# Optimization experiments

Measured on AMD Instinct MI355X. Metric: run time of the kernel, lower is better.

Reference implementation:

```python
import jax, jax.numpy as jnp
import numpy as np

B, S, HID = 2, 2048, 1024
NH, HD = 16, 64  # num heads, head dim
NEG = 1e10

def setup_inputs() -> dict:
    key = jax.random.key(0)
    ks = jax.random.split(key, 4)
    scale = 1.0 / np.sqrt(HID)
    return {
        "hidden_states": jax.random.normal(ks[0], (B, S, HID), jnp.float32),
        "attention_mask": jnp.zeros((B, 1, 1, S), jnp.float32),
        "Wq": jax.random.normal(ks[1], (HID, HID), jnp.float32) * scale,
        "bq": jnp.zeros((HID,), jnp.float32),
        "Wk": jax.random.normal(ks[2], (HID, HID), jnp.float32) * scale,
        "bk": jnp.zeros((HID,), jnp.float32),
        "Wv": jax.random.normal(ks[3], (HID, HID), jnp.float32) * scale,
        "bv": jnp.zeros((HID,), jnp.float32),
    }

def _split_heads(x):
    # [B,S,HID] -> [B,NH,S,HD]
    return x.reshape(B, S, NH, HD).transpose(0, 2, 1, 3)

def reference(hidden_states, attention_mask, Wq, bq, Wk, bk, Wv, bv):
    q = _split_heads(hidden_states @ Wq.T + bq)
    k = _split_heads(hidden_states @ Wk.T + bk)
    v = _split_heads(hidden_states @ Wv.T + bv)
    scores = jnp.einsum("bhqd,bhkd->bhqk", q, k) / np.sqrt(HD)
    causal = jnp.tril(jnp.ones((S, S), jnp.float32))  # [S,S]
    scores = scores * causal - NEG * (1.0 - causal)
    scores = scores + attention_mask
    probs = jax.nn.softmax(scores, axis=-1)  # [B,NH,S,S]
    ctx = jnp.einsum("bhqk,bhkd->bhqd", probs, v)
    ctx = ctx.transpose(0, 2, 1, 3).reshape(B, S, HID)
    return (ctx, probs)
```

## Files before the change

kernel.cpp:

```cpp
#include <hip/hip_runtime.h>

#define S_LEN 2048
#define HIDN  1024
#define NHEAD 16
#define HDIM  64
#define NBATCH 2

typedef __bf16 bf16x8 __attribute__((ext_vector_type(8)));
typedef float  f32x4  __attribute__((ext_vector_type(4)));
typedef unsigned int  u32x4 __attribute__((ext_vector_type(4)));
typedef unsigned short u16;
typedef unsigned short u16x4 __attribute__((ext_vector_type(4)));

#define LOG2E      1.4426950408889634f
#define QS_L2E     0.18033688011112042f
#define NEG8_L2E  -11.541560327111707f

#define PSTR 68

__device__ __forceinline__ u16 f2bf(float f) {
    union { float f; unsigned int u; } v; v.f = f;
    unsigned int u = v.u;
    unsigned int r = ((u >> 16) & 1u) + 0x7FFFu;
    return (u16)((u + r) >> 16);
}

__device__ __forceinline__ f32x4 mfma16(bf16x8 a, bf16x8 b, f32x4 c) {
    return __builtin_amdgcn_mfma_f32_16x16x32_bf16(a, b, c, 0, 0, 0);
}

__device__ __forceinline__ f32x4 zf4() { f32x4 z = {0.f, 0.f, 0.f, 0.f}; return z; }

__device__ __forceinline__ bf16x8 pack8_trunc(f32x4 a, f32x4 b) {
    union { f32x4 f; u32x4 u; } ua, ub;
    ua.f = a; ub.f = b;
    union { unsigned int d[4]; bf16x8 v; } r;
    r.d[0] = __builtin_amdgcn_perm(ua.u.y, ua.u.x, 0x07060302u);
    r.d[1] = __builtin_amdgcn_perm(ua.u.w, ua.u.z, 0x07060302u);
    r.d[2] = __builtin_amdgcn_perm(ub.u.y, ub.u.x, 0x07060302u);
    r.d[3] = __builtin_amdgcn_perm(ub.u.w, ub.u.z, 0x07060302u);
    return r.v;
}

__device__ __forceinline__ void gld16(void* lds, const void* g) {
    __builtin_amdgcn_global_load_lds(
        (const __attribute__((address_space(1))) void*)g,
        (__attribute__((address_space(3))) void*)lds, 16, 0, 0);
}

__global__ __launch_bounds__(256) void cvt_all(
    const float* __restrict__ hs, const float* __restrict__ Wq,
    const float* __restrict__ Wk, const float* __restrict__ Wv,
    u16* __restrict__ hsb, u16* __restrict__ Wqb,
    u16* __restrict__ Wkb, u16* __restrict__ Wvb)
{
    const int NBH = (NBATCH * S_LEN * HIDN) / 1024;
    const int NBW = (HIDN * HIDN) / 1024;
    int bid = blockIdx.x;
    const float* __restrict__ s; u16* __restrict__ d;
    if (bid < NBH)                { s = hs; d = hsb; }
    else if (bid < NBH + NBW)     { s = Wq; d = Wqb; bid -= NBH; }
    else if (bid < NBH + 2 * NBW) { s = Wk; d = Wkb; bid -= NBH + NBW; }
    else                          { s = Wv; d = Wvb; bid -= NBH + 2 * NBW; }
    const int i = (bid * 256 + (int)threadIdx.x) * 4;
    float4 v = *(const float4*)&s[i];
    u16x4 o = { f2bf(v.x), f2bf(v.y), f2bf(v.z), f2bf(v.w) };
    *(u16x4*)&d[i] = o;
}

__global__ __launch_bounds__(256) void qkv_fused(
    const u16* __restrict__ hsb,
    const u16* __restrict__ Wqb, const u16* __restrict__ Wkb, const u16* __restrict__ Wvb,
    const float* __restrict__ bq, const float* __restrict__ bk, const float* __restrict__ bv,
    u16* __restrict__ Qf, u16* __restrict__ Kf, u16* __restrict__ Vt)
{
    __shared__ u16 As[128 * 64];
    __shared__ u16 Bs[3][64 * 64];

    const int mbase = blockIdx.x * 128;
    const int nbase = blockIdx.y * 64;
    const int tid  = threadIdx.x;
    const int lane = tid & 63;
    const int wv   = tid >> 6;
    const int wm   = wv >> 1, wn = wv & 1;
    const int lrow = lane & 15, quad = lane >> 4;
    const int l7   = lrow & 7;

    const u16* __restrict__ Wm[3] = { Wqb, Wkb, Wvb };

    const u16* ap[4];
#pragma unroll
    for (int t = 0; t < 4; ++t) {
        const int c = tid + t * 256;
        const int r = c >> 3;
        const int o = ((c & 7) ^ (r & 7)) * 8;
        ap[t] = &hsb[(size_t)(mbase + r) * HIDN + o];
    }
    const u16* bp[3][2];
#pragma unroll
    for (int z = 0; z < 3; ++z)
#pragma unroll
        for (int t = 0; t < 2; ++t) {
            const int c = tid + t * 256;
            const int r = c >> 3;
            const int o = ((c & 7) ^ (r & 7)) * 8;
            bp[z][t] = &Wm[z][(size_t)(nbase + r) * HIDN + o];
        }

    f32x4 accqk[2][2][4];
    f32x4 accv[4][2];
#pragma unroll
    for (int z = 0; z < 2; ++z)
#pragma unroll
        for (int j = 0; j < 2; ++j)
#pragma unroll
            for (int i = 0; i < 4; ++i) accqk[z][j][i] = zf4();
#pragma unroll
    for (int i = 0; i < 4; ++i)
#pragma unroll
        for (int j = 0; j < 2; ++j) accv[i][j] = zf4();

    for (int k0 = 0; k0 < HIDN; k0 += 64) {
#pragma unroll
        for (int t = 0; t < 4; ++t)
            gld16(&As[(tid + t * 256) * 8], ap[t] + k0);
#pragma unroll
        for (int z = 0; z < 3; ++z)
#pragma unroll
            for (int t = 0; t < 2; ++t)
                gld16(&Bs[z][(tid + t * 256) * 8], bp[z][t] + k0);
        __syncthreads();

#pragma unroll
        for (int kk = 0; kk < 2; ++kk) {
            const int sc = ((kk * 4 + quad) ^ l7) * 8;
            bf16x8 hf[4], wf[3][2];
#pragma unroll
            for (int i = 0; i < 4; ++i)
                hf[i] = *(const bf16x8*)&As[(wm * 64 + i * 16 + lrow) * 64 + sc];
#pragma unroll
            for (int z = 0; z < 3; ++z)
#pragma unroll
                for (int j = 0; j < 2; ++j)
                    wf[z][j] = *(const bf16x8*)&Bs[z][(wn * 32 + j * 16 + lrow) * 64 + sc];
#pragma unroll
            for (int z = 0; z < 2; ++z)
#pragma unroll
                for (int j = 0; j < 2; ++j)
#pragma unroll
                    for (int i = 0; i < 4; ++i)
                        accqk[z][j][i] = mfma16(wf[z][j], hf[i], accqk[z][j][i]);
#pragma unroll
            for (int i = 0; i < 4; ++i)
#pragma unroll
                for (int j = 0; j < 2; ++j)
                    accv[i][j] = mfma16(hf[i], wf[2][j], accv[i][j]);
        }
        __syncthreads();
    }

#pragma unroll
    for (int z = 0; z < 2; ++z) {
        u16* __restrict__ O = (z == 0) ? Qf : Kf;
        const float* __restrict__ bias = (z == 0) ? bq : bk;
#pragma unroll
        for (int j = 0; j < 2; ++j) {
#pragma unroll
            for (int i = 0; i < 4; ++i) {
                const int n0 = nbase + wn * 32 + j * 16 + quad * 4;
                const int m  = mbase + wm * 64 + i * 16 + lrow;
                const float4 b4 = *(const float4*)&bias[n0];
                u16x4 pk = { f2bf(accqk[z][j][i][0] + b4.x), f2bf(accqk[z][j][i][1] + b4.y),
                             f2bf(accqk[z][j][i][2] + b4.z), f2bf(accqk[z][j][i][3] + b4.w) };
                *(u16x4*)&O[(size_t)m * HIDN + n0] = pk;
            }
        }
    }
    {
        const int bb = mbase >> 11;
        const int sb = mbase & 2047;
#pragma unroll
        for (int i = 0; i < 4; ++i) {
#pragma unroll
            for (int j = 0; j < 2; ++j) {
                const int n = nbase + wn * 32 + j * 16 + lrow;
                const int hh = n >> 6, d = n & 63;
                const float bs = bv[n];
                const int s0 = sb + wm * 64 + i * 16 + quad * 4;
                u16x4 pk = { f2bf(accv[i][j][0] + bs), f2bf(accv[i][j][1] + bs),
                             f2bf(accv[i][j][2] + bs), f2bf(accv[i][j][3] + bs) };
                *(u16x4*)&Vt[(((size_t)(bb * NHEAD + hh)) * HDIM + d) * S_LEN + s0] = pk;
            }
        }
    }
}

__global__ __launch_bounds__(256) void attn_kernel(
    const u16* __restrict__ Qf,
    const u16* __restrict__ Kf,
    const u16* __restrict__ Vt,
    const float* __restrict__ amask,
    float* __restrict__ ctx,
    float* __restrict__ probs)
{
    const int qt = 127 - blockIdx.x;
    const int h  = blockIdx.y;
    const int b  = blockIdx.z;
    const int bh = b * NHEAD + h;
    const int tid  = threadIdx.x;
    const int lane = tid & 63;
    const int wv   = tid >> 6;
    const int lrow = lane & 15, quad = lane >> 4;
    const int row0 = qt * 16;
    const int dti  = qt >> 2;
    const int nkt  = dti + 1;

    __shared__ float pfl[4][16 * PSTR];
    __shared__ float l_sh[4][16];

    {
        const int tail  = nkt * 64;
        const int nt4   = (S_LEN - tail) >> 2;
        const int r  = tid >> 4;
        const int c0 = tid & 15;
        const f32x4 zf = {0.f, 0.f, 0.f, 0.f};
        float* pr = &probs[((size_t)bh * S_LEN + row0 + r) * S_LEN + tail];
        for (int c4 = c0; c4 < nt4; c4 += 16)
            __builtin_nontemporal_store(zf, (f32x4*)&pr[c4 * 4]);
    }

    const u16* qp = &Qf[((size_t)b * S_LEN + row0 + lrow) * HIDN + h * HDIM + quad * 8];
    const bf16x8 qa0 = *(const bf16x8*)qp;
    const bf16x8 qa1 = *(const bf16x8*)(qp + 32);

    const float* __restrict__ am = &amask[(size_t)b * S_LEN];
    const u16* __restrict__ kbase = &Kf[(size_t)b * S_LEN * HIDN + h * HDIM + quad * 8];

    float l_lane[4] = {0.f, 0.f, 0.f, 0.f};
    for (int kt = wv; kt < nkt; kt += 4) {
        f32x4 c[4];
#pragma unroll
        for (int cb = 0; cb < 4; ++cb) {
            const int col = kt * 64 + cb * 16 + lrow;
            const u16* kp = kbase + (size_t)col * HIDN;
            bf16x8 kb0 = *(const bf16x8*)kp;
            bf16x8 kb1 = *(const bf16x8*)(kp + 32);
            c[cb] = mfma16(qa0, kb0, zf4());
            c[cb] = mfma16(qa1, kb1, c[cb]);
        }
        if (kt == dti) {
#pragma unroll
            for (int cb = 0; cb < 4; ++cb) {
                const int col = kt * 64 + cb * 16 + lrow;
                const float m8 = fmaf(am[col], LOG2E, NEG8_L2E);
#pragma unroll
                for (int reg = 0; reg < 4; ++reg) {
                    const int row = row0 + quad * 4 + reg;
                    const float e = exp2f(fmaf(c[cb][reg], QS_L2E, m8));
                    l_lane[reg] += (col <= row) ? e : 0.f;
                }
            }
        } else {
#pragma unroll
            for (int cb = 0; cb < 4; ++cb) {
                const int col = kt * 64 + cb * 16 + lrow;
                const float m8 = fmaf(am[col], LOG2E, NEG8_L2E);
#pragma unroll
                for (int reg = 0; reg < 4; ++reg)
                    l_lane[reg] += exp2f(fmaf(c[cb][reg], QS_L2E, m8));
            }
        }
    }
#pragma unroll
    for (int reg = 0; reg < 4; ++reg) {
#pragma unroll
        for (int off = 1; off < 16; off <<= 1)
            l_lane[reg] += __shfl_xor(l_lane[reg], off, 16);
    }
    if (lrow == 0) {
#pragma unroll
        for (int reg = 0; reg < 4; ++reg)
            l_sh[wv][quad * 4 + reg] = l_lane[reg];
    }
    __syncthreads();
    float inv_l[4];
#pragma unroll
    for (int reg = 0; reg < 4; ++reg) {
        const int rr = quad * 4 + reg;
        inv_l[reg] = 1.f / (l_sh[0][rr] + l_sh[1][rr] + l_sh[2][rr] + l_sh[3][rr]);
    }

    f32x4 av[4];
#pragma unroll
    for (int db = 0; db < 4; ++db) av[db] = zf4();

    float* __restrict__ pw = pfl[wv];
    const u16* __restrict__ vbase = &Vt[(size_t)bh * HDIM * S_LEN + quad * 8];

    for (int kt = wv; kt < nkt; kt += 4) {
        f32x4 c[4];
#pragma unroll
        for (int cb = 0; cb < 4; ++cb) {
            const int col = kt * 64 + cb * 16 + lrow;
            const u16* kp = kbase + (size_t)col * HIDN;
            bf16x8 kb0 = *(const bf16x8*)kp;
            bf16x8 kb1 = *(const bf16x8*)(kp + 32);
            c[cb] = mfma16(qa0, kb0, zf4());
            c[cb] = mfma16(qa1, kb1, c[cb]);
        }
        if (kt == dti) {
#pragma unroll
            for (int cb = 0; cb < 4; ++cb) {
                const int col = kt * 64 + cb * 16 + lrow;
                const float m8 = fmaf(am[col], LOG2E, NEG8_L2E);
#pragma unroll
                for (int reg = 0; reg < 4; ++reg) {
                    const int row = row0 + quad * 4 + reg;
                    const float p = (col <= row)
                        ? exp2f(fmaf(c[cb][reg], QS_L2E, m8)) * inv_l[reg] : 0.f;
                    pw[(quad * 4 + reg) * PSTR + cb * 16 + lrow] = p;
                }
            }
        } else {
#pragma unroll
            for (int cb = 0; cb < 4; ++cb) {
                const int col = kt * 64 + cb * 16 + lrow;
                const float m8 = fmaf(am[col], LOG2E, NEG8_L2E);
#pragma unroll
                for (int reg = 0; reg < 4; ++reg) {
                    const float p = exp2f(fmaf(c[cb][reg], QS_L2E, m8)) * inv_l[reg];
                    pw[(quad * 4 + reg) * PSTR + cb * 16 + lrow] = p;
                }
            }
        }

#pragma unroll
        for (int it = 0; it < 4; ++it) {
            const int r = it * 4 + quad;
            f32x4 v = *(const f32x4*)&pw[r * PSTR + lrow * 4];
            __builtin_nontemporal_store(
                v, (f32x4*)&probs[((size_t)bh * S_LEN + row0 + r) * S_LEN + kt * 64 + lrow * 4]);
        }

        f32x4 p0 = *(const f32x4*)&pw[lrow * PSTR + quad * 8];
        f32x4 p1 = *(const f32x4*)&pw[lrow * PSTR + quad * 8 + 4];
        f32x4 p2 = *(const f32x4*)&pw[lrow * PSTR + 32 + quad * 8];
        f32x4 p3 = *(const f32x4*)&pw[lrow * PSTR + 32 + quad * 8 + 4];
        bf16x8 pa0 = pack8_trunc(p0, p1);
        bf16x8 pa1 = pack8_trunc(p2, p3);
#pragma unroll
        for (int db = 0; db < 4; ++db) {
            const u16* vp = vbase + (size_t)(db * 16 + lrow) * S_LEN + kt * 64;
            bf16x8 vb0 = *(const bf16x8*)vp;
            bf16x8 vb1 = *(const bf16x8*)(vp + 32);
            av[db] = mfma16(pa0, vb0, av[db]);
            av[db] = mfma16(pa1, vb1, av[db]);
        }
    }

#pragma unroll
    for (int db = 0; db < 4; ++db)
#pragma unroll
        for (int reg = 0; reg < 4; ++reg)
            pw[lane * 16 + ((db * 4 + reg + (lane >> 1)) & 15)] = av[db][reg];
    __syncthreads();
#pragma unroll
    for (int reg = 0; reg < 4; ++reg) {
        const int sl = lane * 16 + ((wv * 4 + reg + (lane >> 1)) & 15);
        const float s = pfl[0][sl] + pfl[1][sl] + pfl[2][sl] + pfl[3][sl];
        __builtin_nontemporal_store(
            s, &ctx[((size_t)b * S_LEN + row0 + quad * 4 + reg) * HIDN + h * HDIM + wv * 16 + lrow]);
    }
}

extern "C" void kernel_launch(void* const* d_in, const int* in_sizes, int n_in,
                              void* d_out, int out_size, void* d_ws, size_t ws_size,
                              hipStream_t stream)
{
    const float* hs    = (const float*)d_in[0];
    const float* amask = (const float*)d_in[1];
    const float* Wq    = (const float*)d_in[2];
    const float* bq    = (const float*)d_in[3];
    const float* Wk    = (const float*)d_in[4];
    const float* bk    = (const float*)d_in[5];
    const float* Wv    = (const float*)d_in[6];
    const float* bv    = (const float*)d_in[7];

    float* out   = (float*)d_out;
    float* ctx   = out;
    float* probs = out + (size_t)NBATCH * S_LEN * HIDN;

    const size_t NTOK = (size_t)NBATCH * S_LEN;
    u16* hsb = (u16*)d_ws;
    u16* Wqb = hsb + NTOK * HIDN;
    u16* Wkb = Wqb + (size_t)HIDN * HIDN;
    u16* Wvb = Wkb + (size_t)HIDN * HIDN;
    u16* Qf  = Wvb + (size_t)HIDN * HIDN;
    u16* Kf  = Qf + NTOK * HIDN;
    u16* Vt  = Kf + NTOK * HIDN;

    const int nblk_cvt = (int)(NTOK * HIDN / 1024) + 3 * (HIDN * HIDN / 1024);
    cvt_all<<<nblk_cvt, 256, 0, stream>>>(hs, Wq, Wk, Wv, hsb, Wqb, Wkb, Wvb);

    qkv_fused<<<dim3(32, 16), 256, 0, stream>>>(hsb, Wqb, Wkb, Wvb, bq, bk, bv, Qf, Kf, Vt);
    attn_kernel<<<dim3(128, 16, 2), 256, 0, stream>>>(Qf, Kf, Vt, amask, ctx, probs);
}
```

Before: 762.1 us.

## Cache bf16 exp scores in LDS to avoid recomputing QK^T in second pass

The first pass now stores unnormalized exponentials as bf16 in shared memory. The second pass reuses them to write normalized probabilities and feed the PV MFMA, instead of recomputing QK^T and exp. Normalization of the context is applied after accumulation. The launch is split into two kernels with different LDS footprints depending on how many key tiles each query tile needs. This trades large LDS use (lower occupancy) and bf16 rounding of stored probabilities for less compute and K-loading.

```diff
diff --git a/kernel.cpp b/kernel.cpp
--- a/kernel.cpp
+++ b/kernel.cpp
@@ -16,8 +16,6 @@
 #define QS_L2E     0.18033688011112042f
 #define NEG8_L2E  -11.541560327111707f
 
-#define PSTR 68
-
 __device__ __forceinline__ u16 f2bf(float f) {
     union { float f; unsigned int u; } v; v.f = f;
     unsigned int u = v.u;
@@ -25,22 +23,16 @@
     return (u16)((u + r) >> 16);
 }
 
+__device__ __forceinline__ float bf2f(u16 h) {
+    union { unsigned int u; float f; } v; v.u = ((unsigned int)h) << 16;
+    return v.f;
+}
+
 __device__ __forceinline__ f32x4 mfma16(bf16x8 a, bf16x8 b, f32x4 c) {
     return __builtin_amdgcn_mfma_f32_16x16x32_bf16(a, b, c, 0, 0, 0);
 }
 
 __device__ __forceinline__ f32x4 zf4() { f32x4 z = {0.f, 0.f, 0.f, 0.f}; return z; }
-
-__device__ __forceinline__ bf16x8 pack8_trunc(f32x4 a, f32x4 b) {
-    union { f32x4 f; u32x4 u; } ua, ub;
-    ua.f = a; ub.f = b;
-    union { unsigned int d[4]; bf16x8 v; } r;
-    r.d[0] = __builtin_amdgcn_perm(ua.u.y, ua.u.x, 0x07060302u);
-    r.d[1] = __builtin_amdgcn_perm(ua.u.w, ua.u.z, 0x07060302u);
-    r.d[2] = __builtin_amdgcn_perm(ub.u.y, ub.u.x, 0x07060302u);
-    r.d[3] = __builtin_amdgcn_perm(ub.u.w, ub.u.z, 0x07060302u);
-    return r.v;
-}
 
 __device__ __forceinline__ void gld16(void* lds, const void* g) {
     __builtin_amdgcn_global_load_lds(
@@ -195,15 +187,18 @@
     }
 }
 
-__global__ __launch_bounds__(256) void attn_kernel(
+template<int NC>
+__global__ __launch_bounds__(256) void attn_1p(
     const u16* __restrict__ Qf,
     const u16* __restrict__ Kf,
     const u16* __restrict__ Vt,
     const float* __restrict__ amask,
     float* __restrict__ ctx,
-    float* __restrict__ probs)
+    float* __restrict__ probs,
+    int qt_base)
 {
-    const int qt = 127 - blockIdx.x;
+    constexpr int STR = NC + 8;
+    const int qt = qt_base - (int)blockIdx.x;
     const int h  = blockIdx.y;
     const int b  = blockIdx.z;
     const int bh = b * NHEAD + h;
@@ -215,7 +210,7 @@
     const int dti  = qt >> 2;
     const int nkt  = dti + 1;
 
-    __shared__ float pfl[4][16 * PSTR];
+    __shared__ __align__(16) u16 expb[16 * STR];
     __shared__ float l_sh[4][16];
 
     {
@@ -256,8 +251,10 @@
 #pragma unroll
                 for (int reg = 0; reg < 4; ++reg) {
                     const int row = row0 + quad * 4 + reg;
-                    const float e = exp2f(fmaf(c[cb][reg], QS_L2E, m8));
-                    l_lane[reg] += (col <= row) ? e : 0.f;
+                    const float e = (col <= row)
+                        ? exp2f(fmaf(c[cb][reg], QS_L2E, m8)) : 0.f;
+                    l_lane[reg] += e;
+                    expb[(quad * 4 + reg) * STR + kt * 64 + cb * 16 + lrow] = f2bf(e);
                 }
             }
         } else {
@@ -266,8 +263,11 @@
                 const int col = kt * 64 + cb * 16 + lrow;
                 const float m8 = fmaf(am[col], LOG2E, NEG8_L2E);
 #pragma unroll
-                for (int reg = 0; reg < 4; ++reg)
-                    l_lane[reg] += exp2f(fmaf(c[cb][reg], QS_L2E, m8));
+                for (int reg = 0; reg < 4; ++reg) {
+                    const float e = exp2f(fmaf(c[cb][reg], QS_L2E, m8));
+                    l_lane[reg] += e;
+                    expb[(quad * 4 + reg) * STR + kt * 64 + cb * 16 + lrow] = f2bf(e);
+                }
             }
         }
     }
@@ -294,60 +294,22 @@
 #pragma unroll
     for (int db = 0; db < 4; ++db) av[db] = zf4();
 
-    float* __restrict__ pw = pfl[wv];
     const u16* __restrict__ vbase = &Vt[(size_t)bh * HDIM * S_LEN + quad * 8];
 
     for (int kt = wv; kt < nkt; kt += 4) {
-        f32x4 c[4];
-#pragma unroll
-        for (int cb = 0; cb < 4; ++cb) {
-            const int col = kt * 64 + cb * 16 + lrow;
-            const u16* kp = kbase + (size_t)col * HIDN;
-            bf16x8 kb0 = *(const bf16x8*)kp;
-            bf16x8 kb1 = *(const bf16x8*)(kp + 32);
-            c[cb] = mfma16(qa0, kb0, zf4());
-            c[cb] = mfma16(qa1, kb1, c[cb]);
-        }
-        if (kt == dti) {
-#pragma unroll
-            for (int cb = 0; cb < 4; ++cb) {
-                const int col = kt * 64 + cb * 16 + lrow;
-                const float m8 = fmaf(am[col], LOG2E, NEG8_L2E);
-#pragma unroll
-                for (int reg = 0; reg < 4; ++reg) {
-                    const int row = row0 + quad * 4 + reg;
-                    const float p = (col <= row)
-                        ? exp2f(fmaf(c[cb][reg], QS_L2E, m8)) * inv_l[reg] : 0.f;
-                    pw[(quad * 4 + reg) * PSTR + cb * 16 + lrow] = p;
-                }
-            }
-        } else {
-#pragma unroll
-            for (int cb = 0; cb < 4; ++cb) {
-                const int col = kt * 64 + cb * 16 + lrow;
-                const float m8 = fmaf(am[col], LOG2E, NEG8_L2E);
-#pragma unroll
-                for (int reg = 0; reg < 4; ++reg) {
-                    const float p = exp2f(fmaf(c[cb][reg], QS_L2E, m8)) * inv_l[reg];
-                    pw[(quad * 4 + reg) * PSTR + cb * 16 + lrow] = p;
-                }
-            }
-        }
-
 #pragma unroll
         for (int it = 0; it < 4; ++it) {
-            const int r = it * 4 + quad;
-            f32x4 v = *(const f32x4*)&pw[r * PSTR + lrow * 4];
+            const int r = quad * 4 + it;
+            const float inv = inv_l[it];
+            u16x4 p4 = *(const u16x4*)&expb[r * STR + kt * 64 + lrow * 4];
+            f32x4 o;
+#pragma unroll
+            for (int j = 0; j < 4; ++j) o[j] = bf2f(p4[j]) * inv;
             __builtin_nontemporal_store(
-                v, (f32x4*)&probs[((size_t)bh * S_LEN + row0 + r) * S_LEN + kt * 64 + lrow * 4]);
-        }
-
-        f32x4 p0 = *(const f32x4*)&pw[lrow * PSTR + quad * 8];
-        f32x4 p1 = *(const f32x4*)&pw[lrow * PSTR + quad * 8 + 4];
-        f32x4 p2 = *(const f32x4*)&pw[lrow * PSTR + 32 + quad * 8];
-        f32x4 p3 = *(const f32x4*)&pw[lrow * PSTR + 32 + quad * 8 + 4];
-        bf16x8 pa0 = pack8_trunc(p0, p1);
-        bf16x8 pa1 = pack8_trunc(p2, p3);
+                o, (f32x4*)&probs[((size_t)bh * S_LEN + row0 + r) * S_LEN + kt * 64 + lrow * 4]);
+        }
+        const bf16x8 pa0 = *(const bf16x8*)&expb[lrow * STR + kt * 64 + quad * 8];
+        const bf16x8 pa1 = *(const bf16x8*)&expb[lrow * STR + kt * 64 + 32 + quad * 8];
 #pragma unroll
         for (int db = 0; db < 4; ++db) {
             const u16* vp = vbase + (size_t)(db * 16 + lrow) * S_LEN + kt * 64;
@@ -357,17 +319,25 @@
             av[db] = mfma16(pa1, vb1, av[db]);
         }
     }
-
 #pragma unroll
     for (int db = 0; db < 4; ++db)
 #pragma unroll
         for (int reg = 0; reg < 4; ++reg)
-            pw[lane * 16 + ((db * 4 + reg + (lane >> 1)) & 15)] = av[db][reg];
+            av[db][reg] *= inv_l[reg];
+
     __syncthreads();
+    float* cmb = (float*)expb;
+#pragma unroll
+    for (int db = 0; db < 4; ++db)
+#pragma unroll
+        for (int reg = 0; reg < 4; ++reg)
+            cmb[wv * (64 * 17) + lane * 17 + db * 4 + reg] = av[db][reg];
+    __syncthreads();
 #pragma unroll
     for (int reg = 0; reg < 4; ++reg) {
-        const int sl = lane * 16 + ((wv * 4 + reg + (lane >> 1)) & 15);
-        const float s = pfl[0][sl] + pfl[1][sl] + pfl[2][sl] + pfl[3][sl];
+        const int sl = lane * 17 + wv * 4 + reg;
+        const float s = cmb[0 * (64 * 17) + sl] + cmb[1 * (64 * 17) + sl]
+                      + cmb[2 * (64 * 17) + sl] + cmb[3 * (64 * 17) + sl];
         __builtin_nontemporal_store(
             s, &ctx[((size_t)b * S_LEN + row0 + quad * 4 + reg) * HIDN + h * HDIM + wv * 16 + lrow]);
     }
@@ -403,5 +373,7 @@
     cvt_all<<<nblk_cvt, 256, 0, stream>>>(hs, Wq, Wk, Wv, hsb, Wqb, Wkb, Wvb);
 
     qkv_fused<<<dim3(32, 16), 256, 0, stream>>>(hsb, Wqb, Wkb, Wvb, bq, bk, bv, Qf, Kf, Vt);
-    attn_kernel<<<dim3(128, 16, 2), 256, 0, stream>>>(Qf, Kf, Vt, amask, ctx, probs);
-}
+
+    attn_1p<2048><<<dim3(64, 16, 2), 256, 0, stream>>>(Qf, Kf, Vt, amask, ctx, probs, 127);
+    attn_1p<1024><<<dim3(64, 16, 2), 256, 0, stream>>>(Qf, Kf, Vt, amask, ctx, probs, 63);
+}
```

After: 701.2 us. -8.0%, faster.
